# Kernel tuning notes

Hardware: AMD Instinct MI355X
Metric: run time of the kernel (lower is better)

Reference implementation:

```python
import jax, jax.numpy as jnp
import numpy as np

H, D = 4, 64  # num_heads, hidden_feats
IN_FEATS, OUT_FEATS = 1, 128
N_NODES, N_EDGES = 100000, 1600000
NEG_SLOPE = 0.2  # DGL GATConv default


def setup_inputs() -> dict:
    key = jax.random.key(0)
    ks = jax.random.split(key, 9)
    features = jax.random.normal(ks[0], (N_NODES, IN_FEATS), dtype=jnp.float32)
    src = jax.random.randint(ks[1], (N_EDGES,), 0, N_NODES)
    dst = jax.random.randint(ks[2], (N_EDGES,), 0, N_NODES)
    # GATConv params
    W = jax.random.normal(ks[3], (IN_FEATS, H * D), dtype=jnp.float32) * 0.5
    attn_l = jax.random.normal(ks[4], (H, D), dtype=jnp.float32) * 0.1
    attn_r = jax.random.normal(ks[5], (H, D), dtype=jnp.float32) * 0.1
    bias_gat = jnp.zeros((H * D,), dtype=jnp.float32)
    # fc params
    fc_W = jax.random.normal(ks[6], (H * D, OUT_FEATS), dtype=jnp.float32) * 0.05
    fc_b = jax.random.normal(ks[7], (OUT_FEATS,), dtype=jnp.float32) * 0.01
    return {"features": features, "W": W, "attn_l": attn_l, "attn_r": attn_r,
            "bias_gat": bias_gat, "fc_W": fc_W, "fc_b": fc_b,
            "src": src, "dst": dst}


def reference(features, W, attn_l, attn_r, bias_gat, fc_W, fc_b, src, dst):
    N = features.shape[0]
    # linear projection -> [N, H, D]
    feat = (features @ W).reshape(N, H, D)
    # per-node attention terms [N, H]
    el = jnp.einsum('nhd,hd->nh', feat, attn_l)
    er = jnp.einsum('nhd,hd->nh', feat, attn_r)
    # per-edge scores [E, H]
    e = jax.nn.leaky_relu(el[src] + er[dst], NEG_SLOPE)
    # segment softmax over incoming edges of each dst node
    emax = jax.ops.segment_max(e, dst, num_segments=N)  # [N, H]
    ee = jnp.exp(e - emax[dst])
    denom = jax.ops.segment_sum(ee, dst, num_segments=N)  # [N, H]
    alpha = ee / denom[dst]  # [E, H]
    # attention-weighted aggregation: scatter-add messages to dst
    msg = alpha[:, :, None] * feat[src]  # [E, H, D]
    rst = jax.ops.segment_sum(msg, dst, num_segments=N)  # [N, H, D]
    rst = rst + bias_gat.reshape(1, H, D)
    h = rst.reshape(N, H * D)
    out = h @ fc_W + fc_b  # [N, OUT_FEATS]
    return out.mean(axis=0)  # [OUT_FEATS]
```

## Files before the change

### kernel.cpp

```cpp
#include <hip/hip_runtime.h>

#define NEG_SLOPE 0.2f

#define GB_SHIFT 9
#define GB_NODES 512
#define GCAP 9216
#define NBLK 512
#define MAXB 256
#define SCHUNK 4096

#define DESC_OFF 1024
#define REC_OFF  (DESC_OFF + NBLK * MAXB * 4)


__global__ __launch_bounds__(256) void k_place(const int* __restrict__ src,
                                               const int* __restrict__ dst,
                                               int* __restrict__ desc,
                                               unsigned* __restrict__ rec,
                                               float* __restrict__ hdr,
                                               int E, int nbins, int chunk) {
    __shared__ unsigned      raw[SCHUNK];
    __shared__ unsigned char binb[SCHUNK];
    __shared__ unsigned      sorted[SCHUNK];
    __shared__ int hist[MAXB], startS[MAXB], cur[MAXB];

    int tid = threadIdx.x, blk = blockIdx.x;
    if (blk == 0 && tid < 16) hdr[tid] = 0.f;
    hist[tid] = 0;
    __syncthreads();

    int lo = blk * chunk;
    int hi = lo + chunk; if (hi > E) hi = E;
    int tot = hi - lo;

    for (int i = tid; i < tot; i += 256) {
        int d = dst[lo + i], s = src[lo + i];
        int b = d >> GB_SHIFT;
        raw[i]  = ((unsigned)(d & (GB_NODES - 1)) << 17) | (unsigned)s;
        binb[i] = (unsigned char)b;
        atomicAdd(&hist[b], 1);
    }
    __syncthreads();

    int h = hist[tid];
    startS[tid] = h;
    __syncthreads();
    for (int d = 1; d < 256; d <<= 1) {
        int t = (tid >= d) ? startS[tid - d] : 0;
        __syncthreads();
        startS[tid] += t;
        __syncthreads();
    }
    int ex = startS[tid] - h;
    __syncthreads();
    startS[tid] = ex;
    cur[tid] = ex;
    __syncthreads();

    for (int i = tid; i < tot; i += 256) {
        int p = atomicAdd(&cur[binb[i]], 1);
        sorted[p] = raw[i];
    }
    __syncthreads();

    size_t base = (size_t)blk * SCHUNK;
    for (int i = tid; i < tot; i += 256)
        rec[base + i] = sorted[i];
    desc[(size_t)blk * MAXB + tid] = (startS[tid] << 16) | hist[tid];
}

__global__ __launch_bounds__(512) void k_gather(const float* __restrict__ f,
                                                const float* __restrict__ W,
                                                const float* __restrict__ attn_l,
                                                const float* __restrict__ attn_r,
                                                const int* __restrict__ desc,
                                                const unsigned* __restrict__ rec,
                                                float* __restrict__ S_sum,
                                                int N) {
    __shared__ float par[8];
    __shared__ int   deg[GB_NODES];
    __shared__ int   startS[GB_NODES];
    __shared__ int   scanB[GB_NODES];
    __shared__ int   cur[GB_NODES];
    __shared__ int   segst[NBLK];
    __shared__ int   segcnt[NBLK];
    __shared__ float sortedf[GCAP];

    int tid = threadIdx.x;
    int bin = blockIdx.x, nbase = bin << GB_SHIFT;

    if (tid < 256) {
        float w  = W[tid];
        float vl = w * attn_l[tid];
        float vr = w * attn_r[tid];
        #pragma unroll
        for (int off = 32; off > 0; off >>= 1) {
            vl += __shfl_down(vl, off, 64);
            vr += __shfl_down(vr, off, 64);
        }
        if ((tid & 63) == 0) {
            int hh = tid >> 6;
            par[hh]     = vl;
            par[4 + hh] = vr;
        }
    }
    deg[tid] = 0;
    {
        int dsc = desc[(size_t)tid * MAXB + bin];
        segst[tid]  = dsc >> 16;
        segcnt[tid] = dsc & 0xFFFF;
    }
    __syncthreads();

    float al[4], ar[4];
    #pragma unroll
    for (int h = 0; h < 4; ++h) { al[h] = par[h]; ar[h] = par[4 + h]; }

    {
        const unsigned* r0 = rec + (size_t)tid * SCHUNK + segst[tid];
        int c = segcnt[tid];
        for (int i = 0; i < c; ++i)
            atomicAdd(&deg[r0[i] >> 17], 1);
    }
    __syncthreads();

    scanB[tid] = deg[tid];
    __syncthreads();
    for (int d = 1; d < GB_NODES; d <<= 1) {
        int t = (tid >= d) ? scanB[tid - d] : 0;
        __syncthreads();
        scanB[tid] += t;
        __syncthreads();
    }
    int ex = scanB[tid] - deg[tid];
    startS[tid] = ex;
    cur[tid] = ex;
    __syncthreads();

    {
        const unsigned* r0 = rec + (size_t)tid * SCHUNK + segst[tid];
        int c = segcnt[tid];
        for (int i = 0; i < c; ++i) {
            unsigned rc = r0[i];
            int p = atomicAdd(&cur[rc >> 17], 1);
            if (p < GCAP) sortedf[p] = f[rc & 0x1FFFF];
        }
    }
    __syncthreads();

    int st  = startS[tid];
    int len = deg[tid];
    int en  = st + len; if (en > GCAP) en = GCAP; if (st > GCAP) st = GCAP;
    float fd = (len > 0) ? f[nbase + tid] : 0.f;

    float dn[4] = {0.f, 0.f, 0.f, 0.f};
    float nm[4] = {0.f, 0.f, 0.f, 0.f};
    for (int i = st; i < en; ++i) {
        float fs = sortedf[i];
        #pragma unroll
        for (int h = 0; h < 4; ++h) {
            float x = fs * al[h] + fd * ar[h];
            x = (x > 0.f) ? x : NEG_SLOPE * x;
            float ee = __expf(x);
            dn[h] += ee;
            nm[h] += ee * fs;
        }
    }
    float v[4];
    #pragma unroll
    for (int h = 0; h < 4; ++h)
        v[h] = (dn[h] > 0.f) ? nm[h] / dn[h] : 0.f;

    #pragma unroll
    for (int off = 32; off > 0; off >>= 1) {
        #pragma unroll
        for (int h = 0; h < 4; ++h) v[h] += __shfl_down(v[h], off, 64);
    }
    __shared__ float sm[8][4];
    int lane = tid & 63, wave = tid >> 6;
    if (lane == 0) {
        #pragma unroll
        for (int h = 0; h < 4; ++h) sm[wave][h] = v[h];
    }
    __syncthreads();
    if (tid < 4) {
        float s = 0.f;
        #pragma unroll
        for (int w = 0; w < 8; ++w) s += sm[w][tid];
        atomicAdd(&S_sum[tid], s);
    }
}


__global__ void k_prep(const float* __restrict__ W,
                       const float* __restrict__ attn_l,
                       const float* __restrict__ attn_r,
                       float* __restrict__ ws) {
    int tid = threadIdx.x;
    float w  = W[tid];
    float vl = w * attn_l[tid];
    float vr = w * attn_r[tid];
    #pragma unroll
    for (int off = 32; off > 0; off >>= 1) {
        vl += __shfl_down(vl, off, 64);
        vr += __shfl_down(vr, off, 64);
    }
    if ((tid & 63) == 0) {
        int h = tid >> 6;
        ws[h]     = vl;
        ws[4 + h] = vr;
    }
}

__global__ void k_edge(const float* __restrict__ f,
                       const int* __restrict__ src,
                       const int* __restrict__ dst,
                       const float* __restrict__ par,
                       float* __restrict__ denom,
                       float* __restrict__ numer,
                       int E) {
    float al[4], ar[4];
    #pragma unroll
    for (int h = 0; h < 4; ++h) { al[h] = par[h]; ar[h] = par[4 + h]; }
    int stride = gridDim.x * blockDim.x;
    for (int e = blockIdx.x * blockDim.x + threadIdx.x; e < E; e += stride) {
        int s = src[e], d = dst[e];
        float fs = f[s], fd = f[d];
        #pragma unroll
        for (int h = 0; h < 4; ++h) {
            float x = fs * al[h] + fd * ar[h];
            x = (x > 0.f) ? x : NEG_SLOPE * x;
            float ee = __expf(x);
            atomicAdd(&denom[d * 4 + h], ee);
            atomicAdd(&numer[d * 4 + h], ee * fs);
        }
    }
}

__global__ void k_node(const float* __restrict__ denom,
                       const float* __restrict__ numer,
                       float* __restrict__ S_sum,
                       int N) {
    float acc[4] = {0.f, 0.f, 0.f, 0.f};
    int stride = gridDim.x * blockDim.x;
    for (int n = blockIdx.x * blockDim.x + threadIdx.x; n < N; n += stride) {
        float4 dn = *reinterpret_cast<const float4*>(&denom[(size_t)n * 4]);
        float4 nm = *reinterpret_cast<const float4*>(&numer[(size_t)n * 4]);
        acc[0] += (dn.x > 0.f) ? nm.x / dn.x : 0.f;
        acc[1] += (dn.y > 0.f) ? nm.y / dn.y : 0.f;
        acc[2] += (dn.z > 0.f) ? nm.z / dn.z : 0.f;
        acc[3] += (dn.w > 0.f) ? nm.w / dn.w : 0.f;
    }
    #pragma unroll
    for (int off = 32; off > 0; off >>= 1) {
        #pragma unroll
        for (int h = 0; h < 4; ++h) acc[h] += __shfl_down(acc[h], off, 64);
    }
    __shared__ float sm[4][4];
    int lane = threadIdx.x & 63;
    int wave = threadIdx.x >> 6;
    if (lane == 0) {
        #pragma unroll
        for (int h = 0; h < 4; ++h) sm[wave][h] = acc[h];
    }
    __syncthreads();
    if (threadIdx.x < 4) {
        float v = sm[0][threadIdx.x] + sm[1][threadIdx.x]
                + sm[2][threadIdx.x] + sm[3][threadIdx.x];
        atomicAdd(&S_sum[threadIdx.x], v);
    }
}

__global__ __launch_bounds__(512) void k_final(const float* __restrict__ ws,
                                               const float* __restrict__ W,
                                               const float* __restrict__ bias_gat,
                                               const float* __restrict__ fc_W,
                                               const float* __restrict__ fc_b,
                                               float* __restrict__ out,
                                               float invN) {
    __shared__ float sm[4][128];
    int tid = threadIdx.x;
    int o = tid & 127, part = tid >> 7;
    float sp = ws[8 + part] * invN;
    float acc = 0.f;
    #pragma unroll 4
    for (int k = 0; k < 64; ++k) {
        int hd = part * 64 + k;
        float rm = sp * W[hd] + bias_gat[hd];
        acc += rm * fc_W[hd * 128 + o];
    }
    sm[part][o] = acc;
    __syncthreads();
    if (tid < 128)
        out[tid] = sm[0][tid] + sm[1][tid] + sm[2][tid] + sm[3][tid] + fc_b[tid];
}

extern "C" void kernel_launch(void* const* d_in, const int* in_sizes, int n_in,
                              void* d_out, int out_size, void* d_ws, size_t ws_size,
                              hipStream_t stream) {
    const float* features = (const float*)d_in[0];
    const float* W        = (const float*)d_in[1];
    const float* attn_l   = (const float*)d_in[2];
    const float* attn_r   = (const float*)d_in[3];
    const float* bias_gat = (const float*)d_in[4];
    const float* fc_W     = (const float*)d_in[5];
    const float* fc_b     = (const float*)d_in[6];
    const int*   src      = (const int*)d_in[7];
    const int*   dst      = (const int*)d_in[8];
    int N = in_sizes[0];
    int E = in_sizes[7];

    float* ws = (float*)d_ws;
    int nbins = (N + GB_NODES - 1) >> GB_SHIFT;
    int chunk = (E + NBLK - 1) / NBLK;
    size_t need = (size_t)REC_OFF + (size_t)NBLK * SCHUNK * sizeof(unsigned);

    if (nbins <= MAXB && N <= (1 << 17) && chunk <= SCHUNK && ws_size >= need) {
        int* desc     = (int*)((char*)d_ws + DESC_OFF);
        unsigned* rec = (unsigned*)((char*)d_ws + REC_OFF);

        hipLaunchKernelGGL(k_place, dim3(NBLK), dim3(256), 0, stream,
                           src, dst, desc, rec, ws, E, nbins, chunk);
        hipLaunchKernelGGL(k_gather, dim3(nbins), dim3(512), 0, stream,
                           features, W, attn_l, attn_r, desc, rec, ws + 8, N);
    } else {
        float* denom = ws + 16;
        float* numer = denom + (size_t)N * 4;
        size_t zero_bytes = (16 + 2 * (size_t)N * 4) * sizeof(float);
        hipMemsetAsync(d_ws, 0, zero_bytes, stream);
        hipLaunchKernelGGL(k_prep, dim3(1), dim3(256), 0, stream, W, attn_l, attn_r, ws);
        int eb = (E + 255) / 256;
        hipLaunchKernelGGL(k_edge, dim3(eb), dim3(256), 0, stream,
                           features, src, dst, ws, denom, numer, E);
        int nb = (N + 255) / 256;
        if (nb > 2048) nb = 2048;
        hipLaunchKernelGGL(k_node, dim3(nb), dim3(256), 0, stream, denom, numer, ws + 8, N);
    }

    hipLaunchKernelGGL(k_final, dim3(1), dim3(512), 0, stream,
                       ws, W, bias_gat, fc_W, fc_b, (float*)d_out, 1.0f / (float)N);
}
```

Baseline: 52.91 us.

## Stage bin records in LDS once and use wavefront shuffle scans

```diff
diff --git a/kernel.cpp b/kernel.cpp
--- a/kernel.cpp
+++ b/kernel.cpp
@@ -13,7 +13,7 @@
 #define REC_OFF  (DESC_OFF + NBLK * MAXB * 4)
 
 
-__global__ __launch_bounds__(256) void k_place(const int* __restrict__ src,
+__global__ __launch_bounds__(512) void k_place(const int* __restrict__ src,
                                                const int* __restrict__ dst,
                                                int* __restrict__ desc,
                                                unsigned* __restrict__ rec,
@@ -23,17 +23,19 @@
     __shared__ unsigned char binb[SCHUNK];
     __shared__ unsigned      sorted[SCHUNK];
     __shared__ int hist[MAXB], startS[MAXB], cur[MAXB];
+    __shared__ int wtot[4], wpre[4];
 
     int tid = threadIdx.x, blk = blockIdx.x;
+    int lane = tid & 63, wave = tid >> 6;
     if (blk == 0 && tid < 16) hdr[tid] = 0.f;
-    hist[tid] = 0;
+    if (tid < MAXB) hist[tid] = 0;
     __syncthreads();
 
     int lo = blk * chunk;
     int hi = lo + chunk; if (hi > E) hi = E;
     int tot = hi - lo;
 
-    for (int i = tid; i < tot; i += 256) {
+    for (int i = tid; i < tot; i += 512) {
         int d = dst[lo + i], s = src[lo + i];
         int b = d >> GB_SHIFT;
         raw[i]  = ((unsigned)(d & (GB_NODES - 1)) << 17) | (unsigned)s;
@@ -42,31 +44,45 @@
     }
     __syncthreads();
 
-    int h = hist[tid];
-    startS[tid] = h;
-    __syncthreads();
-    for (int d = 1; d < 256; d <<= 1) {
-        int t = (tid >= d) ? startS[tid - d] : 0;
-        __syncthreads();
-        startS[tid] += t;
-        __syncthreads();
-    }
-    int ex = startS[tid] - h;
-    __syncthreads();
-    startS[tid] = ex;
-    cur[tid] = ex;
-    __syncthreads();
-
-    for (int i = tid; i < tot; i += 256) {
+    int h = 0, x = 0;
+    if (tid < MAXB) {
+        h = hist[tid]; x = h;
+        #pragma unroll
+        for (int off = 1; off < 64; off <<= 1) {
+            int y = __shfl_up(x, off, 64);
+            if (lane >= off) x += y;
+        }
+        if (lane == 63) wtot[wave] = x;
+    }
+    __syncthreads();
+    if (tid < 4) {
+        int t = wtot[tid];
+        #pragma unroll
+        for (int off = 1; off < 4; off <<= 1) {
+            int y = __shfl_up(t, off, 64);
+            if (tid >= off) t += y;
+        }
+        wpre[tid] = t - wtot[tid];
+    }
+    __syncthreads();
+    if (tid < MAXB) {
+        int ex = (x - h) + wpre[wave];
+        startS[tid] = ex;
+        cur[tid] = ex;
+    }
+    __syncthreads();
+
+    for (int i = tid; i < tot; i += 512) {
         int p = atomicAdd(&cur[binb[i]], 1);
         sorted[p] = raw[i];
     }
     __syncthreads();
 
     size_t base = (size_t)blk * SCHUNK;
-    for (int i = tid; i < tot; i += 256)
+    for (int i = tid; i < tot; i += 512)
         rec[base + i] = sorted[i];
-    desc[(size_t)blk * MAXB + tid] = (startS[tid] << 16) | hist[tid];
+    if (tid < MAXB)
+        desc[(size_t)blk * MAXB + tid] = (startS[tid] << 16) | hist[tid];
 }
 
 __global__ __launch_bounds__(512) void k_gather(const float* __restrict__ f,
@@ -77,16 +93,14 @@
                                                 const unsigned* __restrict__ rec,
                                                 float* __restrict__ S_sum,
                                                 int N) {
-    __shared__ float par[8];
-    __shared__ int   deg[GB_NODES];
-    __shared__ int   startS[GB_NODES];
-    __shared__ int   scanB[GB_NODES];
-    __shared__ int   cur[GB_NODES];
-    __shared__ int   segst[NBLK];
-    __shared__ int   segcnt[NBLK];
-    __shared__ float sortedf[GCAP];
-
-    int tid = threadIdx.x;
+    __shared__ float    par[8];
+    __shared__ int      deg[GB_NODES], nstart[GB_NODES], ncur[GB_NODES];
+    __shared__ unsigned stageu[GCAP];
+    __shared__ float    sortedf[GCAP];
+    __shared__ int      wtot[8], wpre[8], cntS;
+    __shared__ float    sm[8][4];
+
+    int tid = threadIdx.x, lane = tid & 63, wave = tid >> 6;
     int bin = blockIdx.x, nbase = bin << GB_SHIFT;
 
     if (tid < 256) {
@@ -105,63 +119,97 @@
         }
     }
     deg[tid] = 0;
+
+    int dsc  = desc[(size_t)tid * MAXB + bin];
+    int sst  = dsc >> 16, scnt = dsc & 0xFFFF;
+
+    int x = scnt;
+    #pragma unroll
+    for (int off = 1; off < 64; off <<= 1) {
+        int y = __shfl_up(x, off, 64);
+        if (lane >= off) x += y;
+    }
+    if (lane == 63) wtot[wave] = x;
+    __syncthreads();
+    if (tid < 8) {
+        int t = wtot[tid];
+        #pragma unroll
+        for (int off = 1; off < 8; off <<= 1) {
+            int y = __shfl_up(t, off, 64);
+            if (tid >= off) t += y;
+        }
+        wpre[tid] = t - wtot[tid];
+        if (tid == 7) cntS = t;
+    }
+    __syncthreads();
+    int soff = (x - scnt) + wpre[wave];
+
+    float al[4], ar[4];
+    #pragma unroll
+    for (int h = 0; h < 4; ++h) { al[h] = par[h]; ar[h] = par[4 + h]; }
+
     {
-        int dsc = desc[(size_t)tid * MAXB + bin];
-        segst[tid]  = dsc >> 16;
-        segcnt[tid] = dsc & 0xFFFF;
-    }
-    __syncthreads();
-
-    float al[4], ar[4];
-    #pragma unroll
-    for (int h = 0; h < 4; ++h) { al[h] = par[h]; ar[h] = par[4 + h]; }
-
-    {
-        const unsigned* r0 = rec + (size_t)tid * SCHUNK + segst[tid];
-        int c = segcnt[tid];
-        for (int i = 0; i < c; ++i)
-            atomicAdd(&deg[r0[i] >> 17], 1);
-    }
-    __syncthreads();
-
-    scanB[tid] = deg[tid];
-    __syncthreads();
-    for (int d = 1; d < GB_NODES; d <<= 1) {
-        int t = (tid >= d) ? scanB[tid - d] : 0;
-        __syncthreads();
-        scanB[tid] += t;
-        __syncthreads();
-    }
-    int ex = scanB[tid] - deg[tid];
-    startS[tid] = ex;
-    cur[tid] = ex;
-    __syncthreads();
-
-    {
-        const unsigned* r0 = rec + (size_t)tid * SCHUNK + segst[tid];
-        int c = segcnt[tid];
-        for (int i = 0; i < c; ++i) {
+        const unsigned* r0 = rec + (size_t)tid * SCHUNK + sst;
+        for (int i = 0; i < scnt; ++i) {
             unsigned rc = r0[i];
-            int p = atomicAdd(&cur[rc >> 17], 1);
-            if (p < GCAP) sortedf[p] = f[rc & 0x1FFFF];
-        }
-    }
-    __syncthreads();
-
-    int st  = startS[tid];
+            int p = soff + i;
+            if (p < GCAP) {
+                stageu[p] = rc;
+                atomicAdd(&deg[rc >> 17], 1);
+            }
+        }
+    }
+    __syncthreads();
+    int cnt = cntS; if (cnt > GCAP) cnt = GCAP;
+
+    int dv = deg[tid];
+    int x2 = dv;
+    #pragma unroll
+    for (int off = 1; off < 64; off <<= 1) {
+        int y = __shfl_up(x2, off, 64);
+        if (lane >= off) x2 += y;
+    }
+    if (lane == 63) wtot[wave] = x2;
+    __syncthreads();
+    if (tid < 8) {
+        int t = wtot[tid];
+        #pragma unroll
+        for (int off = 1; off < 8; off <<= 1) {
+            int y = __shfl_up(t, off, 64);
+            if (tid >= off) t += y;
+        }
+        wpre[tid] = t - wtot[tid];
+    }
+    __syncthreads();
+    int ex = (x2 - dv) + wpre[wave];
+    nstart[tid] = ex;
+    ncur[tid]   = ex;
+    __syncthreads();
+
+    for (int i = tid; i < cnt; i += 512) {
+        unsigned rc = stageu[i];
+        int p = atomicAdd(&ncur[rc >> 17], 1);
+        if (p < GCAP) sortedf[p] = f[rc & 0x1FFFF];
+    }
+    __syncthreads();
+
+    int st  = nstart[tid];
     int len = deg[tid];
     int en  = st + len; if (en > GCAP) en = GCAP; if (st > GCAP) st = GCAP;
     float fd = (len > 0) ? f[nbase + tid] : 0.f;
 
     float dn[4] = {0.f, 0.f, 0.f, 0.f};
     float nm[4] = {0.f, 0.f, 0.f, 0.f};
+    float br[4];
+    #pragma unroll
+    for (int h = 0; h < 4; ++h) br[h] = fd * ar[h];
     for (int i = st; i < en; ++i) {
         float fs = sortedf[i];
         #pragma unroll
         for (int h = 0; h < 4; ++h) {
-            float x = fs * al[h] + fd * ar[h];
-            x = (x > 0.f) ? x : NEG_SLOPE * x;
-            float ee = __expf(x);
+            float xx = fmaf(fs, al[h], br[h]);
+            xx = (xx > 0.f) ? xx : NEG_SLOPE * xx;
+            float ee = __expf(xx);
             dn[h] += ee;
             nm[h] += ee * fs;
         }
@@ -176,8 +224,6 @@
         #pragma unroll
         for (int h = 0; h < 4; ++h) v[h] += __shfl_down(v[h], off, 64);
     }
-    __shared__ float sm[8][4];
-    int lane = tid & 63, wave = tid >> 6;
     if (lane == 0) {
         #pragma unroll
         for (int h = 0; h < 4; ++h) sm[wave][h] = v[h];
@@ -319,7 +365,7 @@
         int* desc     = (int*)((char*)d_ws + DESC_OFF);
         unsigned* rec = (unsigned*)((char*)d_ws + REC_OFF);
 
-        hipLaunchKernelGGL(k_place, dim3(NBLK), dim3(256), 0, stream,
+        hipLaunchKernelGGL(k_place, dim3(NBLK), dim3(512), 0, stream,
                            src, dst, desc, rec, ws, E, nbins, chunk);
         hipLaunchKernelGGL(k_gather, dim3(nbins), dim3(512), 0, stream,
                            features, W, attn_l, attn_r, desc, rec, ws + 8, N);
```

New measurement: 48.50 us. -8.3%, faster.
